# Performance work log

Measured on AMD Instinct MI355X. Metric: run time of the kernel, lower is better.

Reference implementation:

```python
import jax, jax.numpy as jnp
import numpy as np

N_EMBD = 1024
N_HEAD = 16
STRIDE = 128
C = 8
SEQ = 2048
BATCH = 2


def _sparse_causal_mask(nd, ns, stride, c, dtype):
    # Faithful vectorization of _sparse_attention_mask:
    # column j is globally visible if (j % stride) >= stride - c (the last c
    # columns of each stride block), each query also sees its own stride block,
    # and everything is causally masked (j <= q).
    j = jnp.arange(ns)
    q = jnp.arange(ns)[:, None]
    col_sel = (j % stride) >= (stride - c)          # strided summary columns
    same_block = (j[None, :] // stride) == (q // stride)  # local block
    causal = j[None, :] <= q
    mask = ((col_sel[None, :] | same_block) & causal).astype(dtype)
    return mask[ns - nd:]


def setup_inputs() -> dict:
    key = jax.random.key(0)
    k1, k2, k3 = jax.random.split(key, 3)
    inputs = jax.random.normal(k1, (BATCH, SEQ, N_EMBD), dtype=jnp.float32)
    w_attn = jax.random.normal(k2, (N_EMBD, 3 * N_EMBD), dtype=jnp.float32) * 0.02
    b_attn = jnp.zeros((3 * N_EMBD,), dtype=jnp.float32)
    proj_std = 0.02 / np.sqrt(2 * 24)  # n_layer = 24
    w_proj = jax.random.normal(k3, (N_EMBD, N_EMBD), dtype=jnp.float32) * proj_std
    b_proj = jnp.zeros((N_EMBD,), dtype=jnp.float32)
    return {"inputs": inputs, "w_attn": w_attn, "b_attn": b_attn,
            "w_proj": w_proj, "b_proj": b_proj}


def reference(inputs, w_attn, b_attn, w_proj, b_proj):
    B, S, E = inputs.shape
    H = N_HEAD
    D = E // H
    qkv = inputs @ w_attn + b_attn                     # [B,S,3E]
    q, k, v = jnp.split(qkv, 3, axis=-1)
    def split_heads(x):
        return x.reshape(B, S, H, D).transpose(0, 2, 1, 3)  # [B,H,S,D]
    q, k, v = split_heads(q), split_heads(k), split_heads(v)
    present = jnp.stack([k, v], axis=1)                # [B,2,H,S,D]
    scale = jnp.asarray(D, q.dtype) ** 0.5
    w = jnp.einsum('bhqd,bhkd->bhqk', q, k) / scale    # [B,H,S,S]
    mask = _sparse_causal_mask(S, S, STRIDE, C, w.dtype)
    w = w * mask - 1e10 * (1.0 - mask)
    p = jax.nn.softmax(w, axis=-1).astype(v.dtype)
    h = jnp.einsum('bhqk,bhkd->bhqd', p, v)            # [B,H,S,D]
    h = h.transpose(0, 2, 1, 3).reshape(B, S, E)       # merge heads
    h = h @ w_proj + b_proj
    # dropout p=0.0 (eval) -> identity
    return (h, present)
```

## Files before the change

### kernel.cpp

```cpp
#include <hip/hip_runtime.h>
#include <stdint.h>

typedef unsigned short u16;
typedef unsigned int u32;
typedef __attribute__((ext_vector_type(4))) float f32x4;
typedef __attribute__((ext_vector_type(4))) u16 u16x4;
typedef __attribute__((ext_vector_type(8))) __bf16 bf16x8;

__device__ __forceinline__ u16 f2bf(float f) {
  u32 u = __builtin_bit_cast(u32, f);
  u = (u + 0x7FFFu + ((u >> 16) & 1u)) >> 16;
  return (u16)u;
}

__device__ __forceinline__ void gload_lds16(const void* g, void* l) {
  __builtin_amdgcn_global_load_lds(
      (const __attribute__((address_space(1))) void*)(uintptr_t)(g),
      (__attribute__((address_space(3))) void*)(u32)(uintptr_t)(l),
      16, 0, 0);
}

__global__ __launch_bounds__(256) void k_prep(
    const float* __restrict__ x, u16* __restrict__ xbf,
    const float* __restrict__ wa, u16* __restrict__ wat,
    const float* __restrict__ wp, u16* __restrict__ wpt) {
  __shared__ float tile[32][33];
  const int bid = blockIdx.x, t = threadIdx.x;
  if (bid < 4096) {
    int i = bid * 256 + t;
    f32x4 v = ((const f32x4*)x)[i];
    u16x4 o = { f2bf(v.x), f2bf(v.y), f2bf(v.z), f2bf(v.w) };
    ((u16x4*)xbf)[i] = o;
    return;
  }
  const float* in;
  u16* out;
  int n0, k0, N;
  if (bid < 4096 + 3072) {
    int idx = bid - 4096;
    in = wa; out = wat; N = 3072;
    n0 = (idx % 96) * 32; k0 = (idx / 96) * 32;
  } else {
    int idx = bid - 7168;
    in = wp; out = wpt; N = 1024;
    n0 = (idx & 31) * 32; k0 = (idx >> 5) * 32;
  }
  int c = t & 31, r0 = t >> 5;
#pragma unroll
  for (int i = 0; i < 4; ++i)
    tile[r0 + i * 8][c] = in[(size_t)(k0 + r0 + i * 8) * N + n0 + c];
  __syncthreads();
  int on = t >> 3, ok = (t & 7) * 4;
  u16x4 o = { f2bf(tile[ok + 0][on]), f2bf(tile[ok + 1][on]),
              f2bf(tile[ok + 2][on]), f2bf(tile[ok + 3][on]) };
  *(u16x4*)&out[(size_t)(n0 + on) * 1024 + k0 + ok] = o;
}

__global__ __launch_bounds__(256) void k_kv(const float* __restrict__ present,
                                            u16* __restrict__ kbf,
                                            u16* __restrict__ vtw) {
  __shared__ float tile[32][33];
  const int bid = blockIdx.x, t = threadIdx.x;
  if (bid >= 4096) {
    int i = bid - 4096;
    size_t idx = (size_t)i * 256 + t;
    size_t b = idx >> 19, off = idx & ((1u << 19) - 1);
    f32x4 v = ((const f32x4*)present)[b * (1u << 20) + off];
    u16x4 o = { f2bf(v.x), f2bf(v.y), f2bf(v.z), f2bf(v.w) };
    ((u16x4*)kbf)[idx] = o;
    return;
  }
  int bh = bid >> 7, rem = bid & 127;
  int s0 = (rem >> 1) * 32, d0 = (rem & 1) * 32;
  int b = bh >> 4, h = bh & 15;
  const float* vsrc = present + (((size_t)(b * 2 + 1) * 16 + h) * 2048) * 64;
  u16* vdst = vtw + ((size_t)bh * 64) * 2048;
  int c = t & 31, r0 = t >> 5;
#pragma unroll
  for (int i = 0; i < 4; ++i)
    tile[r0 + i * 8][c] = vsrc[(size_t)(s0 + r0 + i * 8) * 64 + d0 + c];
  __syncthreads();
  int on = t >> 3, ok = (t & 7) * 4;
  u16x4 o = { f2bf(tile[ok + 0][on]), f2bf(tile[ok + 1][on]),
              f2bf(tile[ok + 2][on]), f2bf(tile[ok + 3][on]) };
  *(u16x4*)&vdst[(size_t)(d0 + on) * 2048 + s0 + ok] = o;
}

__global__ __launch_bounds__(512, 1) void k_gemm256(
    const u16* __restrict__ A, const u16* __restrict__ Bt,
    const float* __restrict__ bias, u16* __restrict__ outq,
    float* __restrict__ outp) {
  __shared__ u16 a_lds[2][256 * 64];
  __shared__ u16 b_lds[2][192 * 64];
  const int t = threadIdx.x;
  const int lane = t & 63, w = t >> 6;
  const int cc = lane & 15, g = lane >> 4;
  const int wr = w >> 2, wc = w & 3;

  int f = blockIdx.y * 16 + blockIdx.x;
  int xcd = f & 7, idx = f >> 3;
  const int m0 = ((xcd >> 1) * 4 + (idx >> 3)) * 256;
  const int n0 = ((xcd & 1) * 8 + (idx & 7)) * 192;

  const int srow = t >> 3;
  const int scolb = (t & 7) * 16;
  const size_t pitch = 2048;

  auto stageB = [&](int bi, int kt) {
#pragma unroll
    for (int i = 0; i < 3; ++i) {
      int row = i * 64 + srow;
      gload_lds16((const char*)Bt + (size_t)(n0 + row) * pitch + kt * 128 +
                      (scolb ^ ((row & 7) << 4)),
                  (char*)b_lds[bi] + row * 128 + scolb);
    }
  };
  auto stageA = [&](int bi, int kt) {
#pragma unroll
    for (int i = 0; i < 4; ++i) {
      int row = i * 64 + srow;
      gload_lds16((const char*)A + (size_t)(m0 + row) * pitch + kt * 128 +
                      (scolb ^ ((row & 7) << 4)),
                  (char*)a_lds[bi] + row * 128 + scolb);
    }
  };

  f32x4 acc[8][3] = {};

  stageB(0, 0);
  stageA(0, 0);

  for (int j = 0; j < 16; ++j) {
    const int bi = j & 1, nx = bi ^ 1;
    if (j < 15) {
      stageB(nx, j + 1);
      asm volatile("s_waitcnt vmcnt(3)\n\ts_barrier" ::: "memory");
    } else {
      asm volatile("s_waitcnt vmcnt(0)\n\ts_barrier" ::: "memory");
    }

    bf16x8 bfr[3][2];
#pragma unroll
    for (int nf = 0; nf < 3; ++nf) {
      int row = wc * 48 + nf * 16 + cc;
#pragma unroll
      for (int kk = 0; kk < 2; ++kk)
        bfr[nf][kk] = *(const bf16x8*)((const char*)b_lds[bi] + row * 128 +
                                       ((kk * 64 + g * 16) ^ ((row & 7) << 4)));
    }
#pragma unroll
    for (int q = 0; q < 2; ++q) {
      bf16x8 af[2][2];
#pragma unroll
      for (int mf = 0; mf < 2; ++mf) {
        int row = wr * 128 + q * 32 + mf * 16 + cc;
#pragma unroll
        for (int kk = 0; kk < 2; ++kk)
          af[mf][kk] = *(const bf16x8*)((const char*)a_lds[bi] + row * 128 +
                                        ((kk * 64 + g * 16) ^ ((row & 7) << 4)));
      }
      __builtin_amdgcn_s_setprio(1);
#pragma unroll
      for (int mf = 0; mf < 2; ++mf)
#pragma unroll
        for (int nf = 0; nf < 3; ++nf)
#pragma unroll
          for (int kk = 0; kk < 2; ++kk)
            acc[q * 2 + mf][nf] = __builtin_amdgcn_mfma_f32_16x16x32_bf16(
                af[mf][kk], bfr[nf][kk], acc[q * 2 + mf][nf], 0, 0, 0);
      __builtin_amdgcn_s_setprio(0);
    }

    if (j < 15) stageA(nx, j + 1);

#pragma unroll
    for (int q = 2; q < 4; ++q) {
      bf16x8 af[2][2];
#pragma unroll
      for (int mf = 0; mf < 2; ++mf) {
        int row = wr * 128 + q * 32 + mf * 16 + cc;
#pragma unroll
        for (int kk = 0; kk < 2; ++kk)
          af[mf][kk] = *(const bf16x8*)((const char*)a_lds[bi] + row * 128 +
                                        ((kk * 64 + g * 16) ^ ((row & 7) << 4)));
      }
      __builtin_amdgcn_s_setprio(1);
#pragma unroll
      for (int mf = 0; mf < 2; ++mf)
#pragma unroll
        for (int nf = 0; nf < 3; ++nf)
#pragma unroll
          for (int kk = 0; kk < 2; ++kk)
            acc[q * 2 + mf][nf] = __builtin_amdgcn_mfma_f32_16x16x32_bf16(
                af[mf][kk], bfr[nf][kk], acc[q * 2 + mf][nf], 0, 0, 0);
      __builtin_amdgcn_s_setprio(0);
    }

    if (j < 15)
      asm volatile("s_waitcnt vmcnt(4)\n\ts_barrier" ::: "memory");
  }

  float bv[3];
#pragma unroll
  for (int nf = 0; nf < 3; ++nf) bv[nf] = bias[n0 + wc * 48 + nf * 16 + cc];

#pragma unroll
  for (int mf = 0; mf < 8; ++mf)
#pragma unroll
    for (int nf = 0; nf < 3; ++nf) {
      int n = n0 + wc * 48 + nf * 16 + cc;
      int mb = m0 + wr * 128 + mf * 16 + g * 4;
      float v[4];
#pragma unroll
      for (int j = 0; j < 4; ++j) v[j] = acc[mf][nf][j] + bv[nf];
      if (n < 1024) {
#pragma unroll
        for (int j = 0; j < 4; ++j) outq[(size_t)(mb + j) * 1024 + n] = f2bf(v[j]);
      } else {
        int n2 = n - 1024;
        int kv = n2 >> 10; n2 &= 1023;
        int hh = n2 >> 6, d = n2 & 63;
        int bb = mb >> 11, ss = mb & 2047;
        float* pr = outp + ((((size_t)bb * 2 + kv) * 16 + hh) * 2048 + ss) * 64 + d;
#pragma unroll
        for (int j = 0; j < 4; ++j) pr[(size_t)j * 64] = v[j];
      }
    }
}

template <int EPI, int BN>
__global__ __launch_bounds__(256) void k_gemm(
    const u16* __restrict__ A, const u16* __restrict__ Bt,
    const float* __restrict__ bias, u16* __restrict__ outq,
    float* __restrict__ outp, int M, int N, int K) {
  __shared__ u16 a_lds[128 * 64];
  __shared__ u16 b_lds[BN * 64];
  const int t = threadIdx.x;
  const int lane = t & 63, w = t >> 6;

  int m0, n0;
  {
    constexpr int NXT = (EPI == 0) ? 24 : 16;
    constexpr int NCH = (EPI == 0) ? 12 : 8;
    int f = blockIdx.y * NXT + blockIdx.x;
    int xcd = f & 7, idx = f >> 3;
    int mt = (xcd >> 1) * 8 + idx / NCH;
    int nt = (xcd & 1) * NCH + idx % NCH;
    m0 = mt * 128;
    n0 = nt * BN;
  }

  const int srow = t >> 3;
  const int scb = (t & 7) * 16;
  const int ssw = scb ^ ((srow & 7) << 4);
  const size_t pitch = (size_t)K * 2;
  const char* aS = (const char*)A + (size_t)(m0 + srow) * pitch + ssw;
  const char* bS = (const char*)Bt + (size_t)(n0 + srow) * pitch + ssw;
  char* al = (char*)a_lds + t * 16;
  char* bl = (char*)b_lds + t * 16;
  const int wm = (w >> 1) * 64, wn = (w & 1) * (BN / 2);
  const int cc = lane & 15, g = lane >> 4;
  constexpr int NF = BN / 32;

  f32x4 acc[4][NF] = {};

  for (int kt = 0; kt < K; kt += 64) {
    __syncthreads();
#pragma unroll
    for (int i = 0; i < 4; ++i)
      gload_lds16(aS + (size_t)kt * 2 + (size_t)i * 32 * pitch, al + i * 4096);
#pragma unroll
    for (int i = 0; i < BN / 32; ++i)
      gload_lds16(bS + (size_t)kt * 2 + (size_t)i * 32 * pitch, bl + i * 4096);
    __syncthreads();
#pragma unroll
    for (int kk = 0; kk < 2; ++kk) {
      bf16x8 af[4], bf_[NF];
#pragma unroll
      for (int mf = 0; mf < 4; ++mf) {
        int row = wm + mf * 16 + cc;
        af[mf] = *(const bf16x8*)((const char*)a_lds + row * 128 +
                                  ((kk * 64 + g * 16) ^ ((row & 7) << 4)));
      }
#pragma unroll
      for (int nf = 0; nf < NF; ++nf) {
        int row = wn + nf * 16 + cc;
        bf_[nf] = *(const bf16x8*)((const char*)b_lds + row * 128 +
                                   ((kk * 64 + g * 16) ^ ((row & 7) << 4)));
      }
#pragma unroll
      for (int mf = 0; mf < 4; ++mf)
#pragma unroll
        for (int nf = 0; nf < NF; ++nf)
          acc[mf][nf] = __builtin_amdgcn_mfma_f32_16x16x32_bf16(
              af[mf], bf_[nf], acc[mf][nf], 0, 0, 0);
    }
  }

  float bv[NF];
#pragma unroll
  for (int nf = 0; nf < NF; ++nf) bv[nf] = bias[n0 + wn + nf * 16 + cc];

#pragma unroll
  for (int mf = 0; mf < 4; ++mf)
#pragma unroll
    for (int nf = 0; nf < NF; ++nf) {
      int n = n0 + wn + nf * 16 + cc;
      int mb = m0 + wm + mf * 16 + g * 4;
      float v[4];
#pragma unroll
      for (int j = 0; j < 4; ++j) v[j] = acc[mf][nf][j] + bv[nf];
      if (EPI == 1) {
#pragma unroll
        for (int j = 0; j < 4; ++j) outp[(size_t)(mb + j) * N + n] = v[j];
      } else if (n < 1024) {
#pragma unroll
        for (int j = 0; j < 4; ++j) outq[(size_t)(mb + j) * 1024 + n] = f2bf(v[j]);
      } else {
        int n2 = n - 1024;
        int kv = n2 >> 10; n2 &= 1023;
        int hh = n2 >> 6, d = n2 & 63;
        int bb = mb >> 11, ss = mb & 2047;
        float* pr = outp + ((((size_t)bb * 2 + kv) * 16 + hh) * 2048 + ss) * 64 + d;
#pragma unroll
        for (int j = 0; j < 4; ++j) pr[(size_t)j * 64] = v[j];
      }
    }
}

__global__ __launch_bounds__(256) void k_attn(
    const u16* __restrict__ qws, const u16* __restrict__ kbf,
    const u16* __restrict__ vtw, u16* __restrict__ hws) {
  const int qb = blockIdx.x, h = blockIdx.y, b = blockIdx.z;
  const int t = threadIdx.x, lane = t & 63, w = t >> 6;
  const int cc = lane & 15, g = lane >> 4;

  __shared__ u16 k_lds[256 * 64];
  __shared__ u16 p_lds[4][32 * 72];
  __shared__ float rsum[4][32];

  const char* kh = (const char*)kbf + (size_t)(b * 16 + h) * (2048 * 128);
  const char* vh = (const char*)vtw + (size_t)(b * 16 + h) * (64 * 4096);

  {
    int rr = t >> 3, seg = (t & 7) * 16;
#pragma unroll
    for (int i = 0; i < 8; ++i) {
      int r = i * 32 + rr;
      int i2 = r - 128;
      int gr = (r < 128) ? (qb * 128 + r) : ((i2 >> 3) * 128 + 120 + (i2 & 7));
      gload_lds16(kh + (size_t)gr * 128 + (seg ^ ((r & 7) << 4)),
                  (char*)k_lds + i * 4096 + t * 16);
    }
  }

  bf16x8 qf_[2][2];
  {
    const char* qsrc = (const char*)qws +
        (size_t)(b * 2048 + qb * 128 + w * 32 + cc) * 2048 + h * 128 + g * 16;
#pragma unroll
    for (int qf = 0; qf < 2; ++qf)
#pragma unroll
      for (int kk = 0; kk < 2; ++kk)
        qf_[qf][kk] = *(const bf16x8*)(qsrc + (size_t)qf * 16 * 2048 + kk * 64);
  }
  __syncthreads();

  const int nsum = 8 * qb;
  f32x4 o_[2][4] = {};
  float lsum[2] = { 0.f, 0.f };

#pragma unroll 2
  for (int ch = 0; ch < 4; ++ch) {
    f32x4 s[4][2] = {};
#pragma unroll
    for (int kf2 = 0; kf2 < 4; ++kf2) {
      int row = ch * 64 + kf2 * 16 + cc;
      const char* kr = (const char*)k_lds + row * 128;
#pragma unroll
      for (int kk = 0; kk < 2; ++kk) {
        bf16x8 kfr = *(const bf16x8*)(kr + ((kk * 64 + g * 16) ^ ((cc & 7) << 4)));
#pragma unroll
        for (int qf = 0; qf < 2; ++qf)
          s[kf2][qf] = __builtin_amdgcn_mfma_f32_16x16x32_bf16(
              kfr, qf_[qf][kk], s[kf2][qf], 0, 0, 0);
      }
    }
#pragma unroll
    for (int qf = 0; qf < 2; ++qf) {
      int q_local = w * 32 + qf * 16 + cc;
#pragma unroll
      for (int kf2 = 0; kf2 < 4; ++kf2) {
#pragma unroll
        for (int j = 0; j < 4; ++j) {
          int key = ch * 64 + kf2 * 16 + g * 4 + j;
          bool vis = (key < 128) ? (key <= q_local) : (key - 128 < nsum);
          float p = vis ? exp2f(s[kf2][qf][j] * 0.180336884f) : 0.f;
          s[kf2][qf][j] = p;
          lsum[qf] += p;
        }
        u16x4 pw = { f2bf(s[kf2][qf][0]), f2bf(s[kf2][qf][1]),
                     f2bf(s[kf2][qf][2]), f2bf(s[kf2][qf][3]) };
        *(u16x4*)&p_lds[w][(qf * 16 + cc) * 72 + kf2 * 16 + g * 4] = pw;
      }
    }
#pragma unroll
    for (int kk = 0; kk < 2; ++kk) {
      bf16x8 pa[2], vb[4];
#pragma unroll
      for (int mf = 0; mf < 2; ++mf)
        pa[mf] = *(const bf16x8*)((const char*)p_lds[w] +
                                  (mf * 16 + cc) * 144 + kk * 64 + g * 16);
      int cb = (ch < 2) ? (qb * 256 + ch * 128 + kk * 64 + g * 16)
                        : (((ch - 2) * 8 + kk * 4 + g) * 256 + 240);
#pragma unroll
      for (int nf = 0; nf < 4; ++nf)
        vb[nf] = *(const bf16x8*)(vh + (size_t)(nf * 16 + cc) * 4096 + cb);
#pragma unroll
      for (int mf = 0; mf < 2; ++mf)
#pragma unroll
        for (int nf = 0; nf < 4; ++nf)
          o_[mf][nf] = __builtin_amdgcn_mfma_f32_16x16x32_bf16(pa[mf], vb[nf],
                                                               o_[mf][nf], 0, 0, 0);
    }
  }

#pragma unroll
  for (int qf = 0; qf < 2; ++qf) {
    float sum = lsum[qf];
    sum += __shfl_xor(sum, 16);
    sum += __shfl_xor(sum, 32);
    if (g == 0) rsum[w][qf * 16 + cc] = sum;
  }
#pragma unroll
  for (int mf = 0; mf < 2; ++mf)
#pragma unroll
    for (int j = 0; j < 4; ++j) {
      float inv = 1.0f / rsum[w][mf * 16 + g * 4 + j];
      size_t row = (size_t)(b * 2048 + qb * 128 + w * 32 + mf * 16 + g * 4 + j);
#pragma unroll
      for (int nf = 0; nf < 4; ++nf)
        hws[row * 1024 + h * 64 + nf * 16 + cc] = f2bf(o_[mf][nf][j] * inv);
    }
}

extern "C" void kernel_launch(void* const* d_in, const int* in_sizes, int n_in,
                              void* d_out, int out_size, void* d_ws, size_t ws_size,
                              hipStream_t stream) {
  const float* x      = (const float*)d_in[0];
  const float* w_attn = (const float*)d_in[1];
  const float* b_attn = (const float*)d_in[2];
  const float* w_proj = (const float*)d_in[3];
  const float* b_proj = (const float*)d_in[4];
  float* h_out   = (float*)d_out;
  float* present = (float*)d_out + 4194304;

  char* ws = (char*)d_ws;
  u16* xbf = (u16*)(ws);
  u16* qws = (u16*)(ws + (8u << 20));
  u16* wat = (u16*)(ws + (16u << 20));
  u16* wpt = (u16*)(ws + (22u << 20));
  u16* kbf = (u16*)(ws + (24u << 20));
  u16* vtw = (u16*)(ws + (32u << 20));
  u16* hws = xbf;

  k_prep<<<8192, 256, 0, stream>>>(x, xbf, w_attn, wat, w_proj, wpt);
  k_gemm256<<<dim3(16, 16), 512, 0, stream>>>(xbf, wat, b_attn, qws, present);
  k_kv<<<8192, 256, 0, stream>>>(present, kbf, vtw);
  k_attn<<<dim3(16, 16, 2), 256, 0, stream>>>(qws, kbf, vtw, hws);
  k_gemm<1, 64><<<dim3(16, 32), 256, 0, stream>>>(hws, wpt, b_proj, nullptr,
                                                  h_out, 4096, 1024, 1024);
}
```

Measured before the change: 87.05 us.

## Interleave next-tile global-to-LDS loads across sub-steps of QKV GEMM loop

Splits staging of the next A tile into two halves and issues the B tile and each A half at the start of separate q sub-steps. All four q sub-steps now run in one loop, with a workgroup barrier after each step. A full vmcnt(0) drain at the end of each k-iteration replaces the earlier partial waits. The goal is to spread memory issue more evenly over the MFMA work, at the cost of more barriers per iteration.

```diff
diff --git a/kernel.cpp b/kernel.cpp
--- a/kernel.cpp
+++ b/kernel.cpp
@@ -115,10 +115,10 @@
                   (char*)b_lds[bi] + row * 128 + scolb);
     }
   };
-  auto stageA = [&](int bi, int kt) {
-#pragma unroll
-    for (int i = 0; i < 4; ++i) {
-      int row = i * 64 + srow;
+  auto stageA2 = [&](int bi, int kt, int half) {
+#pragma unroll
+    for (int i = 0; i < 2; ++i) {
+      int row = (half * 2 + i) * 64 + srow;
       gload_lds16((const char*)A + (size_t)(m0 + row) * pitch + kt * 128 +
                       (scolb ^ ((row & 7) << 4)),
                   (char*)a_lds[bi] + row * 128 + scolb);
@@ -128,28 +128,32 @@
   f32x4 acc[8][3] = {};
 
   stageB(0, 0);
-  stageA(0, 0);
+  stageA2(0, 0, 0);
+  stageA2(0, 0, 1);
+  asm volatile("s_waitcnt vmcnt(0)\n\ts_barrier" ::: "memory");
 
   for (int j = 0; j < 16; ++j) {
     const int bi = j & 1, nx = bi ^ 1;
-    if (j < 15) {
-      stageB(nx, j + 1);
-      asm volatile("s_waitcnt vmcnt(3)\n\ts_barrier" ::: "memory");
-    } else {
-      asm volatile("s_waitcnt vmcnt(0)\n\ts_barrier" ::: "memory");
-    }
 
     bf16x8 bfr[3][2];
 #pragma unroll
-    for (int nf = 0; nf < 3; ++nf) {
-      int row = wc * 48 + nf * 16 + cc;
-#pragma unroll
-      for (int kk = 0; kk < 2; ++kk)
-        bfr[nf][kk] = *(const bf16x8*)((const char*)b_lds[bi] + row * 128 +
-                                       ((kk * 64 + g * 16) ^ ((row & 7) << 4)));
-    }
-#pragma unroll
-    for (int q = 0; q < 2; ++q) {
+    for (int q = 0; q < 4; ++q) {
+      if (j < 15) {
+        if (q == 0) stageB(nx, j + 1);
+        else if (q == 1) stageA2(nx, j + 1, 0);
+        else if (q == 2) stageA2(nx, j + 1, 1);
+      }
+      if (q == 0) {
+#pragma unroll
+        for (int nf = 0; nf < 3; ++nf) {
+          int row = wc * 48 + nf * 16 + cc;
+#pragma unroll
+          for (int kk = 0; kk < 2; ++kk)
+            bfr[nf][kk] =
+                *(const bf16x8*)((const char*)b_lds[bi] + row * 128 +
+                                 ((kk * 64 + g * 16) ^ ((row & 7) << 4)));
+        }
+      }
       bf16x8 af[2][2];
 #pragma unroll
       for (int mf = 0; mf < 2; ++mf) {
@@ -169,35 +173,12 @@
             acc[q * 2 + mf][nf] = __builtin_amdgcn_mfma_f32_16x16x32_bf16(
                 af[mf][kk], bfr[nf][kk], acc[q * 2 + mf][nf], 0, 0, 0);
       __builtin_amdgcn_s_setprio(0);
-    }
-
-    if (j < 15) stageA(nx, j + 1);
-
-#pragma unroll
-    for (int q = 2; q < 4; ++q) {
-      bf16x8 af[2][2];
-#pragma unroll
-      for (int mf = 0; mf < 2; ++mf) {
-        int row = wr * 128 + q * 32 + mf * 16 + cc;
-#pragma unroll
-        for (int kk = 0; kk < 2; ++kk)
-          af[mf][kk] = *(const bf16x8*)((const char*)a_lds[bi] + row * 128 +
-                                        ((kk * 64 + g * 16) ^ ((row & 7) << 4)));
-      }
-      __builtin_amdgcn_s_setprio(1);
-#pragma unroll
-      for (int mf = 0; mf < 2; ++mf)
-#pragma unroll
-        for (int nf = 0; nf < 3; ++nf)
-#pragma unroll
-          for (int kk = 0; kk < 2; ++kk)
-            acc[q * 2 + mf][nf] = __builtin_amdgcn_mfma_f32_16x16x32_bf16(
-                af[mf][kk], bfr[nf][kk], acc[q * 2 + mf][nf], 0, 0, 0);
-      __builtin_amdgcn_s_setprio(0);
-    }
-
-    if (j < 15)
-      asm volatile("s_waitcnt vmcnt(4)\n\ts_barrier" ::: "memory");
+      if (q < 3) {
+        __builtin_amdgcn_s_barrier();
+      } else if (j < 15) {
+        asm volatile("s_waitcnt vmcnt(0)\n\ts_barrier" ::: "memory");
+      }
+    }
   }
 
   float bv[3];
```

Result: no change. 87.02 us (-0.0%).
